# Kernel optimization log

Measured on AMD Instinct MI355X. Metric: run time of the kernel, lower is better.

The kernel has to match this reference:

```python
import jax, jax.numpy as jnp
import numpy as np

N_NODES = 100000
N_EDGES = 1600000
N_GRAPHS = 512


def _graph_conv(x, W, b, src, dst, n_nodes):
    """DGL GraphConv, norm='both': D_in^-1/2 (A (D_out^-1/2 x)) W + b.
    Weight is applied on the smaller-dim side (same math, less memory)."""
    ones = jnp.ones(src.shape[0], dtype=x.dtype)
    deg_out = jnp.clip(jax.ops.segment_sum(ones, src, num_segments=n_nodes), 1.0)
    deg_in = jnp.clip(jax.ops.segment_sum(ones, dst, num_segments=n_nodes), 1.0)
    h = x * (deg_out ** -0.5)[:, None]
    if W.shape[0] > W.shape[1]:  # reduce feature dim before the SpMM
        h = h @ W
        h = jax.ops.segment_sum(h[src], dst, num_segments=n_nodes)
    else:
        h = jax.ops.segment_sum(h[src], dst, num_segments=n_nodes)
        h = h @ W
    return h * (deg_in ** -0.5)[:, None] + b


def setup_inputs() -> dict:
    key = jax.random.key(0)
    ks = jax.random.split(key, 16)
    x = jax.random.normal(ks[0], (N_NODES, 128), dtype=jnp.float32)
    src = jax.random.randint(ks[1], (N_EDGES,), 0, N_NODES, dtype=jnp.int32)
    dst = jax.random.randint(ks[2], (N_EDGES,), 0, N_NODES, dtype=jnp.int32)
    graph_ids = jnp.sort(jax.random.randint(ks[3], (N_NODES,), 0, N_GRAPHS, dtype=jnp.int32))
    s = 0.05
    return {
        "x": x, "src": src, "dst": dst, "graph_ids": graph_ids,
        "W1": jax.random.normal(ks[4], (128, 256), jnp.float32) * s,
        "b1": jnp.zeros((256,), jnp.float32),
        "W2": jax.random.normal(ks[5], (256, 64), jnp.float32) * s,
        "b2": jnp.zeros((64,), jnp.float32),
        "Wc1": jax.random.normal(ks[6], (64, 18), jnp.float32) * s,
        "bc1": jnp.zeros((18,), jnp.float32),
        "Wc2": jax.random.normal(ks[7], (18, 12), jnp.float32) * s,
        "bc2": jnp.zeros((12,), jnp.float32),
        "Wc3": jax.random.normal(ks[8], (12, 6), jnp.float32) * s,
        "bc3": jnp.zeros((6,), jnp.float32),
        "Wc4": jax.random.normal(ks[9], (6, 2), jnp.float32) * s,
        "bc4": jnp.zeros((2,), jnp.float32),
    }


def reference(x, src, dst, graph_ids, W1, b1, W2, b2, Wc1, bc1, Wc2, bc2, Wc3, bc3, Wc4, bc4):
    n = x.shape[0]
    h = jax.nn.relu(_graph_conv(x, W1, b1, src, dst, n))
    h = jax.nn.relu(_graph_conv(h, W2, b2, src, dst, n))
    # dgl.mean_nodes: per-graph mean over nodes
    sums = jax.ops.segment_sum(h, graph_ids, num_segments=N_GRAPHS)
    cnts = jnp.clip(jax.ops.segment_sum(jnp.ones(n, h.dtype), graph_ids, num_segments=N_GRAPHS), 1.0)
    hg = sums / cnts[:, None]
    # classifier: 4 stacked Linear layers, no activations (faithful to source)
    hg = hg @ Wc1 + bc1
    hg = hg @ Wc2 + bc2
    hg = hg @ Wc3 + bc3
    return hg @ Wc4 + bc4
```

## Files before the change

### kernel.cpp

```cpp
#include <hip/hip_runtime.h>
#include <cstdint>
#include <cstddef>

#define NGRAPHS 512

static inline size_t align_up(size_t x, size_t a){ return (x + a - 1) & ~(a - 1); }

__device__ __forceinline__ unsigned short f2bf(float f){
  unsigned int u = __float_as_uint(f);
  u += 0x7FFFu + ((u >> 16) & 1u);
  return (unsigned short)(u >> 16);
}
__device__ __forceinline__ float bflo(unsigned int u){ return __uint_as_float(u << 16); }
__device__ __forceinline__ float bfhi(unsigned int u){ return __uint_as_float(u & 0xffff0000u); }
__device__ __forceinline__ unsigned int pack2(float a, float b){
  return (unsigned)f2bf(a) | ((unsigned)f2bf(b) << 16);
}

typedef __attribute__((ext_vector_type(8))) short bf16x8;
typedef __attribute__((ext_vector_type(4))) float f32x4;

__global__ __launch_bounds__(256) void k_partcount(const int* __restrict__ src, const int* __restrict__ dst,
                                                   int* __restrict__ cntS, int* __restrict__ cntD, int n_edges){
  __shared__ int cs[256], cd[256];
  int tid = threadIdx.x;
  cs[tid] = 0; cd[tid] = 0;
  __syncthreads();
  int e0 = blockIdx.x * 4096;
  int e1 = min(e0 + 4096, n_edges);
  for (int e = e0 + tid; e < e1; e += 256){
    atomicAdd(&cs[src[e] >> 9], 1);
    atomicAdd(&cd[dst[e] >> 9], 1);
  }
  __syncthreads();
  cntS[blockIdx.x * 256 + tid] = cs[tid];
  cntD[blockIdx.x * 256 + tid] = cd[tid];
}

__global__ __launch_bounds__(256) void k_colscan(int* __restrict__ cntS, int* __restrict__ cntD,
                                                 int* __restrict__ totS, int* __restrict__ totD,
                                                 int nblk, int NB){
  int col = blockIdx.x;
  int* cnt; int* tot; int k;
  if (col < NB){ cnt = cntS; tot = totS; k = col; }
  else         { cnt = cntD; tot = totD; k = col - NB; }
  __shared__ int tsum[256];
  int tid = threadIdx.x;
  int i0 = 2 * tid, i1 = 2 * tid + 1;
  int a = (i0 < nblk) ? cnt[i0 * 256 + k] : 0;
  int b = (i1 < nblk) ? cnt[i1 * 256 + k] : 0;
  int s = a + b;
  tsum[tid] = s;
  __syncthreads();
  for (int off = 1; off < 256; off <<= 1){
    int t = (tid >= off) ? tsum[tid - off] : 0;
    __syncthreads();
    tsum[tid] += t;
    __syncthreads();
  }
  int pre = tsum[tid] - s;
  if (i0 < nblk) cnt[i0 * 256 + k] = pre;
  if (i1 < nblk) cnt[i1 * 256 + k] = pre + a;
  if (tid == 255) tot[k] = tsum[255];
}

__global__ __launch_bounds__(256) void k_scatter_det(const int* __restrict__ src, const int* __restrict__ dst,
                                                     const int* __restrict__ cntS, const int* __restrict__ cntD,
                                                     const int* __restrict__ totS, const int* __restrict__ totD,
                                                     int* __restrict__ baseS, int* __restrict__ baseD,
                                                     int2* __restrict__ pairD, int* __restrict__ srcS,
                                                     int n_edges, int NB){
  __shared__ int s1[256], s2[256], curS[256], curD[256];
  int tid = threadIdx.x;
  int b = blockIdx.x;
  int v1 = (tid < NB) ? totS[tid] : 0;
  int v2 = (tid < NB) ? totD[tid] : 0;
  s1[tid] = v1; s2[tid] = v2;
  __syncthreads();
  for (int off = 1; off < 256; off <<= 1){
    int t1 = (tid >= off) ? s1[tid - off] : 0;
    int t2 = (tid >= off) ? s2[tid - off] : 0;
    __syncthreads();
    s1[tid] += t1; s2[tid] += t2;
    __syncthreads();
  }
  int bS = s1[tid] - v1, bD = s2[tid] - v2;
  if (b == 0 && tid < NB){ baseS[tid] = bS; baseD[tid] = bD; }
  curS[tid] = bS + cntS[b * 256 + tid];
  curD[tid] = bD + cntD[b * 256 + tid];
  __syncthreads();
  int e0 = b * 4096, e1 = min(e0 + 4096, n_edges);
  for (int e = e0 + tid; e < e1; e += 256){
    int s = src[e], d = dst[e];
    int pd = atomicAdd(&curD[d >> 9], 1);
    pairD[pd] = make_int2(s, d);
    int ps = atomicAdd(&curS[s >> 9], 1);
    srcS[ps] = s;
  }
}

__global__ __launch_bounds__(256) void k_bucket_build(const int2* __restrict__ pairD, const int* __restrict__ baseD,
                                                      const int* __restrict__ srcS, const int* __restrict__ baseS,
                                                      int* __restrict__ offs, float* __restrict__ din_s,
                                                      float* __restrict__ dout_s, int* __restrict__ csr_src,
                                                      int NB, int n, int n_edges){
  __shared__ int cd[512], cs[512], cur[512];
  __shared__ int tsum[256];
  int b = blockIdx.x, node0 = b << 9, tid = threadIdx.x;
  int nn = min(512, n - node0);
  for (int i = tid; i < 512; i += 256){ cd[i] = 0; cs[i] = 0; }
  __syncthreads();
  int jd0 = baseD[b], jd1 = (b + 1 < NB) ? baseD[b + 1] : n_edges;
  for (int j = jd0 + tid; j < jd1; j += 256) atomicAdd(&cd[pairD[j].y - node0], 1);
  int js0 = baseS[b], js1 = (b + 1 < NB) ? baseS[b + 1] : n_edges;
  for (int j = js0 + tid; j < js1; j += 256) atomicAdd(&cs[srcS[j] - node0], 1);
  __syncthreads();
  int a0 = cd[2 * tid], a1 = cd[2 * tid + 1];
  int s = a0 + a1;
  tsum[tid] = s;
  __syncthreads();
  for (int off = 1; off < 256; off <<= 1){
    int t = (tid >= off) ? tsum[tid - off] : 0;
    __syncthreads();
    tsum[tid] += t;
    __syncthreads();
  }
  int pre = tsum[tid] - s + jd0;
  cur[2 * tid]     = pre;
  cur[2 * tid + 1] = pre + a0;
  __syncthreads();
  for (int i = tid; i < nn; i += 256){
    offs[node0 + i]   = cur[i];
    din_s[node0 + i]  = 1.0f / sqrtf((float)max(cd[i], 1));
    dout_s[node0 + i] = 1.0f / sqrtf((float)max(cs[i], 1));
  }
  if (b == NB - 1 && tid == 0) offs[n] = n_edges;
  __syncthreads();
  for (int j = jd0 + tid; j < jd1; j += 256){
    int2 e = pairD[j];
    int p = atomicAdd(&cur[e.y - node0], 1);
    csr_src[p] = e.x;
  }
}

__global__ __launch_bounds__(256) void k_prep(const float* __restrict__ x, unsigned int* __restrict__ xb,
                                              long long total4,
                                              const float* __restrict__ W1, unsigned short* __restrict__ Wt1,
                                              const float* __restrict__ W2, unsigned short* __restrict__ Wt2,
                                              float* __restrict__ sums,
                                              const int* __restrict__ gids, int* __restrict__ gb, int n_nodes){
  long long t = (long long)blockIdx.x * 256 + threadIdx.x;
  if (t < total4){
    float4 v = ((const float4*)x)[t];
    xb[t * 2 + 0] = pack2(v.x, v.y);
    xb[t * 2 + 1] = pack2(v.z, v.w);
    return;
  }
  long long u = t - total4;
  if (u < 128 * 256){
    int k = (int)(u / 256), n = (int)(u % 256);
    Wt1[(size_t)n * 128 + k] = f2bf(W1[u]);
    return;
  }
  u -= 128 * 256;
  if (u < 256 * 64){
    int k = (int)(u / 64), n = (int)(u % 64);
    Wt2[(size_t)n * 256 + k] = f2bf(W2[u]);
    return;
  }
  u -= 256 * 64;
  if (u < (long long)NGRAPHS * 64){ sums[u] = 0.f; return; }
  u -= (long long)NGRAPHS * 64;
  if (u < n_nodes){
    int i = (int)u;
    int g  = gids[i];
    int gp = (i > 0) ? gids[i - 1] : -1;
    for (int q = gp + 1; q <= g; ++q) gb[q] = i;
    if (i == n_nodes - 1)
      for (int q = g + 1; q <= NGRAPHS; ++q) gb[q] = n_nodes;
  }
}

__global__ __launch_bounds__(256) void k_spmm1(const unsigned int* __restrict__ xb,
    const int* __restrict__ offs, const int* __restrict__ csr_src,
    const float* __restrict__ dout_s, unsigned int* __restrict__ aggb, int n_nodes){
  int node = (blockIdx.x * blockDim.x + threadIdx.x) >> 5;
  int lane = threadIdx.x & 31;
  if (node >= n_nodes) return;
  int j0 = offs[node], j1 = offs[node + 1];
  const uint2* xp = (const uint2*)xb;
  float4 acc = make_float4(0.f, 0.f, 0.f, 0.f);
  int j = j0;
  for (; j + 4 <= j1; j += 4){
    int s0 = csr_src[j + 0];
    int s1 = csr_src[j + 1];
    int s2 = csr_src[j + 2];
    int s3 = csr_src[j + 3];
    float c0 = dout_s[s0];
    float c1 = dout_s[s1];
    float c2 = dout_s[s2];
    float c3 = dout_s[s3];
    uint2 v0 = xp[(size_t)s0 * 32 + lane];
    uint2 v1 = xp[(size_t)s1 * 32 + lane];
    uint2 v2 = xp[(size_t)s2 * 32 + lane];
    uint2 v3 = xp[(size_t)s3 * 32 + lane];
    acc.x = fmaf(bflo(v0.x), c0, acc.x); acc.y = fmaf(bfhi(v0.x), c0, acc.y);
    acc.z = fmaf(bflo(v0.y), c0, acc.z); acc.w = fmaf(bfhi(v0.y), c0, acc.w);
    acc.x = fmaf(bflo(v1.x), c1, acc.x); acc.y = fmaf(bfhi(v1.x), c1, acc.y);
    acc.z = fmaf(bflo(v1.y), c1, acc.z); acc.w = fmaf(bfhi(v1.y), c1, acc.w);
    acc.x = fmaf(bflo(v2.x), c2, acc.x); acc.y = fmaf(bfhi(v2.x), c2, acc.y);
    acc.z = fmaf(bflo(v2.y), c2, acc.z); acc.w = fmaf(bfhi(v2.y), c2, acc.w);
    acc.x = fmaf(bflo(v3.x), c3, acc.x); acc.y = fmaf(bfhi(v3.x), c3, acc.y);
    acc.z = fmaf(bflo(v3.y), c3, acc.z); acc.w = fmaf(bfhi(v3.y), c3, acc.w);
  }
  for (; j < j1; ++j){
    int s = csr_src[j];
    float sc = dout_s[s];
    uint2 v = xp[(size_t)s * 32 + lane];
    acc.x = fmaf(bflo(v.x), sc, acc.x); acc.y = fmaf(bfhi(v.x), sc, acc.y);
    acc.z = fmaf(bflo(v.y), sc, acc.z); acc.w = fmaf(bfhi(v.y), sc, acc.w);
  }
  uint2 pk;
  pk.x = pack2(acc.x, acc.y);
  pk.y = pack2(acc.z, acc.w);
  ((uint2*)aggb)[(size_t)node * 32 + lane] = pk;
}

#define SCHUNK 4
__global__ __launch_bounds__(256) void k_spmm2_fused(const unsigned short* __restrict__ t2,
    const int* __restrict__ offs, const int* __restrict__ csr_src,
    const float* __restrict__ din_s, const float* __restrict__ b2,
    const int* __restrict__ gb, float* __restrict__ sums){
  __shared__ float bs[64];
  int tid = threadIdx.x;
  int g = blockIdx.x & (NGRAPHS - 1);
  int chunk = blockIdx.x >> 9;
  int hw = chunk * 8 + (tid >> 5);
  int lane = tid & 31;
  if (tid < 64) bs[tid] = 0.f;
  __syncthreads();
  int g0 = gb[g], g1 = gb[g + 1];
  const unsigned int* tp = (const unsigned int*)t2;
  float2 bb = ((const float2*)b2)[lane];
  float sx = 0.f, sy = 0.f;
  for (int node = g0 + hw; node < g1; node += 32){
    int j0 = offs[node], j1 = offs[node + 1];
    float ax = 0.f, ay = 0.f;
    int j = j0;
    for (; j + 4 <= j1; j += 4){
      int s0 = csr_src[j + 0];
      int s1 = csr_src[j + 1];
      int s2 = csr_src[j + 2];
      int s3 = csr_src[j + 3];
      unsigned int v0 = tp[(size_t)s0 * 32 + lane];
      unsigned int v1 = tp[(size_t)s1 * 32 + lane];
      unsigned int v2 = tp[(size_t)s2 * 32 + lane];
      unsigned int v3 = tp[(size_t)s3 * 32 + lane];
      ax += bflo(v0) + bflo(v1) + bflo(v2) + bflo(v3);
      ay += bfhi(v0) + bfhi(v1) + bfhi(v2) + bfhi(v3);
    }
    for (; j < j1; ++j){
      unsigned int v = tp[(size_t)csr_src[j] * 32 + lane];
      ax += bflo(v);
      ay += bfhi(v);
    }
    float ds = din_s[node];
    sx += fmaxf(fmaf(ax, ds, bb.x), 0.f);
    sy += fmaxf(fmaf(ay, ds, bb.y), 0.f);
  }
  atomicAdd(&bs[2 * lane], sx);
  atomicAdd(&bs[2 * lane + 1], sy);
  __syncthreads();
  if (tid < 64) atomicAdd(&sums[(size_t)g * 64 + tid], bs[tid]);
}

template<bool C_BF16, bool EPI, bool EPI2>
__global__ __launch_bounds__(256) void gemm_mfma(
    const unsigned short* __restrict__ A, const unsigned short* __restrict__ Bt, void* __restrict__ Cp,
    int M, int N, int K,
    const float* __restrict__ rowScaleC, const float* __restrict__ rowScaleC2,
    const float* __restrict__ bias){
  constexpr int BM = 128, BN = 64, BK = 32, LDA = 40;
  __shared__ __align__(16) unsigned short As[2][BM * LDA];
  __shared__ __align__(16) unsigned short Bs[2][BN * LDA];
  int tid = threadIdx.x;
  int bm0 = blockIdx.x * BM;
  int bn0 = blockIdx.y * BN;
  int wid = tid >> 6, lane = tid & 63;
  int wm = (wid >> 1) * 64, wn = (wid & 1) * 32;
  int quad = lane >> 4, l16 = lane & 15;
  f32x4 acc[4][2];
#pragma unroll
  for (int t = 0; t < 4; ++t)
#pragma unroll
    for (int u = 0; u < 2; ++u) acc[t][u] = f32x4{0.f, 0.f, 0.f, 0.f};

  uint2 ar[4], br[2];
  auto preload = [&](int kk){
#pragma unroll
    for (int it = 0; it < 4; ++it){
      int i = tid + it * 256;
      int m = i >> 3, c = i & 7;
      int gr = bm0 + m;
      ar[it] = (gr < M) ? *(const uint2*)(A + (size_t)gr * K + kk + c * 4) : make_uint2(0u, 0u);
    }
#pragma unroll
    for (int it = 0; it < 2; ++it){
      int i = tid + it * 256;
      int n = i >> 3, c = i & 7;
      br[it] = *(const uint2*)(Bt + (size_t)(bn0 + n) * K + kk + c * 4);
    }
  };
  auto commit = [&](int buf){
#pragma unroll
    for (int it = 0; it < 4; ++it){
      int i = tid + it * 256;
      int m = i >> 3, c = i & 7;
      *(uint2*)&As[buf][m * LDA + c * 4] = ar[it];
    }
#pragma unroll
    for (int it = 0; it < 2; ++it){
      int i = tid + it * 256;
      int n = i >> 3, c = i & 7;
      *(uint2*)&Bs[buf][n * LDA + c * 4] = br[it];
    }
  };

  preload(0);
  commit(0);
  __syncthreads();
  int nk = K / BK;
  for (int kb = 0; kb < nk; ++kb){
    int cur = kb & 1;
    if (kb + 1 < nk) preload((kb + 1) * BK);
    bf16x8 af[4], bfr[2];
#pragma unroll
    for (int t = 0; t < 4; ++t)
      af[t] = *(const bf16x8*)&As[cur][(wm + t * 16 + l16) * LDA + quad * 8];
#pragma unroll
    for (int u = 0; u < 2; ++u)
      bfr[u] = *(const bf16x8*)&Bs[cur][(wn + u * 16 + l16) * LDA + quad * 8];
#pragma unroll
    for (int t = 0; t < 4; ++t)
#pragma unroll
      for (int u = 0; u < 2; ++u)
        acc[t][u] = __builtin_amdgcn_mfma_f32_16x16x32_bf16(af[t], bfr[u], acc[t][u], 0, 0, 0);
    if (kb + 1 < nk){
      commit(cur ^ 1);
      __syncthreads();
    }
  }
  float bv[2] = {0.f, 0.f};
  if constexpr (EPI){ bv[0] = bias[bn0 + wn + l16]; bv[1] = bias[bn0 + wn + 16 + l16]; }
#pragma unroll
  for (int t = 0; t < 4; ++t){
#pragma unroll
    for (int r = 0; r < 4; ++r){
      int gr = bm0 + wm + t * 16 + quad * 4 + r;
      if (gr < M){
        float rs = 1.f, rs2 = 1.f;
        if constexpr (EPI)  rs  = rowScaleC[gr];
        if constexpr (EPI2) rs2 = rowScaleC2[gr];
#pragma unroll
        for (int u = 0; u < 2; ++u){
          int gc = bn0 + wn + u * 16 + l16;
          float cv = acc[t][u][r];
          if constexpr (EPI)  cv = fmaxf(fmaf(cv, rs, bv[u]), 0.f);
          if constexpr (EPI2) cv *= rs2;
          if constexpr (C_BF16) ((unsigned short*)Cp)[(size_t)gr * N + gc] = f2bf(cv);
          else                  ((float*)Cp)[(size_t)gr * N + gc] = cv;
        }
      }
    }
  }
}

__global__ __launch_bounds__(256) void k_classifier(const float* __restrict__ sums, const int* __restrict__ gb,
    const float* __restrict__ Wc1, const float* __restrict__ bc1,
    const float* __restrict__ Wc2, const float* __restrict__ bc2,
    const float* __restrict__ Wc3, const float* __restrict__ bc3,
    const float* __restrict__ Wc4, const float* __restrict__ bc4,
    float* __restrict__ out){
  __shared__ float w1[64 * 18], w2[18 * 12], w3[12 * 6], w4[6 * 2];
  __shared__ float B1[18], B2[12], B3[6], B4[2];
  int tid = threadIdx.x;
  for (int i = tid; i < 64 * 18; i += 256) w1[i] = Wc1[i];
  for (int i = tid; i < 18 * 12; i += 256) w2[i] = Wc2[i];
  for (int i = tid; i < 12 * 6;  i += 256) w3[i] = Wc3[i];
  for (int i = tid; i < 6 * 2;   i += 256) w4[i] = Wc4[i];
  if (tid < 18) B1[tid] = bc1[tid];
  if (tid < 12) B2[tid] = bc2[tid];
  if (tid < 6)  B3[tid] = bc3[tid];
  if (tid < 2)  B4[tid] = bc4[tid];
  __syncthreads();
  int g = blockIdx.x * 256 + tid;
  float cnt = fmaxf((float)(gb[g + 1] - gb[g]), 1.0f);
  float h[64];
#pragma unroll
  for (int f = 0; f < 64; ++f) h[f] = sums[(size_t)g * 64 + f] / cnt;
  float t1[18];
#pragma unroll
  for (int j = 0; j < 18; ++j){
    float s = B1[j];
    for (int f = 0; f < 64; ++f) s = fmaf(h[f], w1[f * 18 + j], s);
    t1[j] = s;
  }
  float t2[12];
#pragma unroll
  for (int j = 0; j < 12; ++j){
    float s = B2[j];
    for (int f = 0; f < 18; ++f) s = fmaf(t1[f], w2[f * 12 + j], s);
    t2[j] = s;
  }
  float t3[6];
#pragma unroll
  for (int j = 0; j < 6; ++j){
    float s = B3[j];
    for (int f = 0; f < 12; ++f) s = fmaf(t2[f], w3[f * 6 + j], s);
    t3[j] = s;
  }
#pragma unroll
  for (int j = 0; j < 2; ++j){
    float s = B4[j];
    for (int f = 0; f < 6; ++f) s = fmaf(t3[f], w4[f * 2 + j], s);
    out[(size_t)g * 2 + j] = s;
  }
}

extern "C" void kernel_launch(void* const* d_in, const int* in_sizes, int n_in,
                              void* d_out, int out_size, void* d_ws, size_t ws_size,
                              hipStream_t stream){
  const float* x   = (const float*)d_in[0];
  const int*   src = (const int*)d_in[1];
  const int*   dst = (const int*)d_in[2];
  const int*   gid = (const int*)d_in[3];
  const float* W1  = (const float*)d_in[4];
  const float* b1  = (const float*)d_in[5];
  const float* W2  = (const float*)d_in[6];
  const float* b2  = (const float*)d_in[7];
  const float* Wc1 = (const float*)d_in[8];
  const float* bc1 = (const float*)d_in[9];
  const float* Wc2 = (const float*)d_in[10];
  const float* bc2 = (const float*)d_in[11];
  const float* Wc3 = (const float*)d_in[12];
  const float* bc3 = (const float*)d_in[13];
  const float* Wc4 = (const float*)d_in[14];
  const float* bc4 = (const float*)d_in[15];
  float* out = (float*)d_out;

  const int n_nodes = in_sizes[3];
  const int n_edges = in_sizes[1];
  const int F1 = 256, F2 = 64;
  const int NB   = (n_nodes + 511) >> 9;
  const int NBLK = (n_edges + 4095) / 4096;

  char* w = (char*)d_ws;
  size_t o = 0;
  auto alloc = [&](size_t bytes) -> char* {
    char* p = w + o;
    o = align_up(o + bytes, 256);
    return p;
  };
  float* sums      = (float*)alloc((size_t)NGRAPHS * F2 * 4);
  int*   gb        = (int*)  alloc((size_t)(NGRAPHS + 1) * 4);
  int*   cntS      = (int*)  alloc((size_t)NBLK * 256 * 4);
  int*   cntD      = (int*)  alloc((size_t)NBLK * 256 * 4);
  int*   totS      = (int*)  alloc((size_t)256 * 4);
  int*   totD      = (int*)  alloc((size_t)256 * 4);
  int*   baseS     = (int*)  alloc((size_t)256 * 4);
  int*   baseD     = (int*)  alloc((size_t)256 * 4);
  float* dout_s    = (float*)alloc((size_t)n_nodes * 4);
  float* din_s     = (float*)alloc((size_t)n_nodes * 4);
  int*   offs      = (int*)  alloc((size_t)(n_nodes + 1) * 4);
  int*   csr_src   = (int*)  alloc((size_t)n_edges * 4);
  unsigned short* Wt1 = (unsigned short*)alloc((size_t)256 * 128 * 2);
  unsigned short* Wt2 = (unsigned short*)alloc((size_t)64 * 256 * 2);
  unsigned int*   xb  = (unsigned int*)  alloc((size_t)n_nodes * 128 * 2);
  unsigned short* aggb= (unsigned short*)alloc((size_t)n_nodes * 128 * 2);
  unsigned short* h1b = (unsigned short*)alloc((size_t)n_nodes * F1 * 2);
  int2*  pairD = (int2*)aggb;
  int*   srcS  = (int*)((char*)aggb + (size_t)n_edges * 8);
  unsigned short* t2b = aggb;

  {
    long long total4 = (long long)n_nodes * 32;
    long long totalP = total4 + 128 * 256 + 256 * 64 + (long long)NGRAPHS * 64 + n_nodes;
    k_prep<<<(int)((totalP + 255) / 256), 256, 0, stream>>>(x, xb, total4, W1, Wt1, W2, Wt2,
                                                            sums, gid, gb, n_nodes);
  }

  k_partcount   <<<NBLK, 256, 0, stream>>>(src, dst, cntS, cntD, n_edges);
  k_colscan     <<<2 * NB, 256, 0, stream>>>(cntS, cntD, totS, totD, NBLK, NB);
  k_scatter_det <<<NBLK, 256, 0, stream>>>(src, dst, cntS, cntD, totS, totD, baseS, baseD, pairD, srcS, n_edges, NB);
  k_bucket_build<<<NB, 256, 0, stream>>>(pairD, baseD, srcS, baseS, offs, din_s, dout_s, csr_src, NB, n_nodes, n_edges);

  int gx = (n_nodes + 127) / 128;
  {
    long long threads = (long long)n_nodes * 32;
    k_spmm1<<<(int)((threads + 255) / 256), 256, 0, stream>>>(xb, offs, csr_src, dout_s, (unsigned int*)aggb, n_nodes);
    gemm_mfma<true, true, true><<<dim3(gx, F1 / 64), 256, 0, stream>>>(
        aggb, Wt1, h1b, n_nodes, F1, 128, din_s, dout_s, b1);
  }
  {
    gemm_mfma<true, false, false><<<dim3(gx, 1), 256, 0, stream>>>(
        h1b, Wt2, t2b, n_nodes, F2, F1, nullptr, nullptr, nullptr);
    k_spmm2_fused<<<NGRAPHS * SCHUNK, 256, 0, stream>>>(t2b, offs, csr_src, din_s, b2, gb, sums);
  }
  k_classifier<<<NGRAPHS / 256, 256, 0, stream>>>(sums, gb, Wc1, bc1, Wc2, bc2, Wc3, bc3, Wc4, bc4, out);
}
```

Measured before the change: 364.9 us.

## Prescale x by out-degree, software-pipeline gathers, add full-N GEMM1 kernel

Moves the weight, sums and graph-boundary prep into the partcount launch and adds a separate prep kernel that converts x to bf16 already multiplied by dout_s. The SpMM1 inner loop then drops the per-edge dout_s gather and FMAs. Both SpMM gathers are unrolled to 8 with the next batch of indices prefetched. A dedicated GEMM1 kernel keeps the A tile in LDS and loops over all four N tiles, so A is loaded once per block rather than per N-block. The costs are an extra launch, rounding x*s to bf16, more registers in the gather loops, and larger LDS use.

```diff
diff --git a/kernel.cpp b/kernel.cpp
--- a/kernel.cpp
+++ b/kernel.cpp
@@ -21,8 +21,38 @@
 typedef __attribute__((ext_vector_type(4))) float f32x4;
 
 __global__ __launch_bounds__(256) void k_partcount(const int* __restrict__ src, const int* __restrict__ dst,
-                                                   int* __restrict__ cntS, int* __restrict__ cntD, int n_edges){
+                                                   int* __restrict__ cntS, int* __restrict__ cntD, int n_edges, int NBLK,
+                                                   const float* __restrict__ W1, unsigned short* __restrict__ Wt1,
+                                                   const float* __restrict__ W2, unsigned short* __restrict__ Wt2,
+                                                   float* __restrict__ sums,
+                                                   const int* __restrict__ gids, int* __restrict__ gb, int n_nodes){
   __shared__ int cs[256], cd[256];
+  if (blockIdx.x >= NBLK){
+    long long u = (long long)(blockIdx.x - NBLK) * 256 + threadIdx.x;
+    if (u < 128 * 256){
+      int k = (int)(u / 256), n = (int)(u % 256);
+      Wt1[(size_t)n * 128 + k] = f2bf(W1[u]);
+      return;
+    }
+    u -= 128 * 256;
+    if (u < 256 * 64){
+      int k = (int)(u / 64), n = (int)(u % 64);
+      Wt2[(size_t)n * 256 + k] = f2bf(W2[u]);
+      return;
+    }
+    u -= 256 * 64;
+    if (u < (long long)NGRAPHS * 64){ sums[u] = 0.f; return; }
+    u -= (long long)NGRAPHS * 64;
+    if (u < n_nodes){
+      int i = (int)u;
+      int g  = gids[i];
+      int gp = (i > 0) ? gids[i - 1] : -1;
+      for (int q = gp + 1; q <= g; ++q) gb[q] = i;
+      if (i == n_nodes - 1)
+        for (int q = g + 1; q <= NGRAPHS; ++q) gb[q] = n_nodes;
+    }
+    return;
+  }
   int tid = threadIdx.x;
   cs[tid] = 0; cd[tid] = 0;
   __syncthreads();
@@ -143,47 +173,20 @@
   }
 }
 
-__global__ __launch_bounds__(256) void k_prep(const float* __restrict__ x, unsigned int* __restrict__ xb,
-                                              long long total4,
-                                              const float* __restrict__ W1, unsigned short* __restrict__ Wt1,
-                                              const float* __restrict__ W2, unsigned short* __restrict__ Wt2,
-                                              float* __restrict__ sums,
-                                              const int* __restrict__ gids, int* __restrict__ gb, int n_nodes){
+__global__ __launch_bounds__(256) void k_prep2(const float* __restrict__ x,
+                                               const float* __restrict__ dout_s,
+                                               unsigned int* __restrict__ xb, long long total4){
   long long t = (long long)blockIdx.x * 256 + threadIdx.x;
-  if (t < total4){
-    float4 v = ((const float4*)x)[t];
-    xb[t * 2 + 0] = pack2(v.x, v.y);
-    xb[t * 2 + 1] = pack2(v.z, v.w);
-    return;
-  }
-  long long u = t - total4;
-  if (u < 128 * 256){
-    int k = (int)(u / 256), n = (int)(u % 256);
-    Wt1[(size_t)n * 128 + k] = f2bf(W1[u]);
-    return;
-  }
-  u -= 128 * 256;
-  if (u < 256 * 64){
-    int k = (int)(u / 64), n = (int)(u % 64);
-    Wt2[(size_t)n * 256 + k] = f2bf(W2[u]);
-    return;
-  }
-  u -= 256 * 64;
-  if (u < (long long)NGRAPHS * 64){ sums[u] = 0.f; return; }
-  u -= (long long)NGRAPHS * 64;
-  if (u < n_nodes){
-    int i = (int)u;
-    int g  = gids[i];
-    int gp = (i > 0) ? gids[i - 1] : -1;
-    for (int q = gp + 1; q <= g; ++q) gb[q] = i;
-    if (i == n_nodes - 1)
-      for (int q = g + 1; q <= NGRAPHS; ++q) gb[q] = n_nodes;
-  }
+  if (t >= total4) return;
+  float4 v = ((const float4*)x)[t];
+  float s = dout_s[t >> 5];
+  xb[t * 2 + 0] = pack2(v.x * s, v.y * s);
+  xb[t * 2 + 1] = pack2(v.z * s, v.w * s);
 }
 
 __global__ __launch_bounds__(256) void k_spmm1(const unsigned int* __restrict__ xb,
     const int* __restrict__ offs, const int* __restrict__ csr_src,
-    const float* __restrict__ dout_s, unsigned int* __restrict__ aggb, int n_nodes){
+    unsigned int* __restrict__ aggb, int n_nodes){
   int node = (blockIdx.x * blockDim.x + threadIdx.x) >> 5;
   int lane = threadIdx.x & 31;
   if (node >= n_nodes) return;
@@ -191,39 +194,151 @@
   const uint2* xp = (const uint2*)xb;
   float4 acc = make_float4(0.f, 0.f, 0.f, 0.f);
   int j = j0;
-  for (; j + 4 <= j1; j += 4){
-    int s0 = csr_src[j + 0];
-    int s1 = csr_src[j + 1];
-    int s2 = csr_src[j + 2];
-    int s3 = csr_src[j + 3];
-    float c0 = dout_s[s0];
-    float c1 = dout_s[s1];
-    float c2 = dout_s[s2];
-    float c3 = dout_s[s3];
-    uint2 v0 = xp[(size_t)s0 * 32 + lane];
-    uint2 v1 = xp[(size_t)s1 * 32 + lane];
-    uint2 v2 = xp[(size_t)s2 * 32 + lane];
-    uint2 v3 = xp[(size_t)s3 * 32 + lane];
-    acc.x = fmaf(bflo(v0.x), c0, acc.x); acc.y = fmaf(bfhi(v0.x), c0, acc.y);
-    acc.z = fmaf(bflo(v0.y), c0, acc.z); acc.w = fmaf(bfhi(v0.y), c0, acc.w);
-    acc.x = fmaf(bflo(v1.x), c1, acc.x); acc.y = fmaf(bfhi(v1.x), c1, acc.y);
-    acc.z = fmaf(bflo(v1.y), c1, acc.z); acc.w = fmaf(bfhi(v1.y), c1, acc.w);
-    acc.x = fmaf(bflo(v2.x), c2, acc.x); acc.y = fmaf(bfhi(v2.x), c2, acc.y);
-    acc.z = fmaf(bflo(v2.y), c2, acc.z); acc.w = fmaf(bfhi(v2.y), c2, acc.w);
-    acc.x = fmaf(bflo(v3.x), c3, acc.x); acc.y = fmaf(bfhi(v3.x), c3, acc.y);
-    acc.z = fmaf(bflo(v3.y), c3, acc.z); acc.w = fmaf(bfhi(v3.y), c3, acc.w);
+  int nfull = (j1 - j0) >> 3;
+  if (nfull > 0){
+    int idx[8];
+#pragma unroll
+    for (int u = 0; u < 8; ++u) idx[u] = csr_src[j + u];
+    for (int b = 0; b < nfull; ++b){
+      int nidx[8];
+      if (b + 1 < nfull){
+#pragma unroll
+        for (int u = 0; u < 8; ++u) nidx[u] = csr_src[j + 8 + u];
+      }
+      uint2 v[8];
+#pragma unroll
+      for (int u = 0; u < 8; ++u) v[u] = xp[(size_t)idx[u] * 32 + lane];
+#pragma unroll
+      for (int u = 0; u < 8; ++u){
+        acc.x += bflo(v[u].x); acc.y += bfhi(v[u].x);
+        acc.z += bflo(v[u].y); acc.w += bfhi(v[u].y);
+      }
+      if (b + 1 < nfull){
+#pragma unroll
+        for (int u = 0; u < 8; ++u) idx[u] = nidx[u];
+      }
+      j += 8;
+    }
   }
   for (; j < j1; ++j){
-    int s = csr_src[j];
-    float sc = dout_s[s];
-    uint2 v = xp[(size_t)s * 32 + lane];
-    acc.x = fmaf(bflo(v.x), sc, acc.x); acc.y = fmaf(bfhi(v.x), sc, acc.y);
-    acc.z = fmaf(bflo(v.y), sc, acc.z); acc.w = fmaf(bfhi(v.y), sc, acc.w);
+    uint2 v = xp[(size_t)csr_src[j] * 32 + lane];
+    acc.x += bflo(v.x); acc.y += bfhi(v.x);
+    acc.z += bflo(v.y); acc.w += bfhi(v.y);
   }
   uint2 pk;
   pk.x = pack2(acc.x, acc.y);
   pk.y = pack2(acc.z, acc.w);
   ((uint2*)aggb)[(size_t)node * 32 + lane] = pk;
+}
+
+__global__ __launch_bounds__(256) void k_gemm1(const unsigned short* __restrict__ A,
+    const unsigned short* __restrict__ Bt, unsigned short* __restrict__ C,
+    int M, const float* __restrict__ din, const float* __restrict__ dout,
+    const float* __restrict__ bias){
+  constexpr int LDA = 136;
+  __shared__ __align__(16) unsigned short As[128 * LDA];
+  __shared__ __align__(16) unsigned short Bs[64 * LDA];
+  int tid = threadIdx.x;
+  int bm0 = blockIdx.x * 128;
+  int wid = tid >> 6, lane = tid & 63;
+  int wm = wid * 32;
+  int quad = lane >> 4, l16 = lane & 15;
+
+  uint4 areg[8];
+#pragma unroll
+  for (int it = 0; it < 8; ++it){
+    int i = tid + it * 256;
+    int m = i >> 4, c = i & 15;
+    int gr = bm0 + m;
+    areg[it] = (gr < M) ? *(const uint4*)(A + (size_t)gr * 128 + c * 8) : make_uint4(0u, 0u, 0u, 0u);
+  }
+  uint4 breg[4];
+#pragma unroll
+  for (int it = 0; it < 4; ++it){
+    int i = tid + it * 256;
+    int n = i >> 4, c = i & 15;
+    breg[it] = *(const uint4*)(Bt + (size_t)n * 128 + c * 8);
+  }
+#pragma unroll
+  for (int it = 0; it < 8; ++it){
+    int i = tid + it * 256;
+    int m = i >> 4, c = i & 15;
+    *(uint4*)&As[m * LDA + c * 8] = areg[it];
+  }
+#pragma unroll
+  for (int it = 0; it < 4; ++it){
+    int i = tid + it * 256;
+    int n = i >> 4, c = i & 15;
+    *(uint4*)&Bs[n * LDA + c * 8] = breg[it];
+  }
+  float rsv[2][4], rs2v[2][4];
+#pragma unroll
+  for (int t = 0; t < 2; ++t)
+#pragma unroll
+    for (int r = 0; r < 4; ++r){
+      int gr = bm0 + wm + t * 16 + quad * 4 + r;
+      rsv[t][r]  = (gr < M) ? din[gr]  : 0.f;
+      rs2v[t][r] = (gr < M) ? dout[gr] : 0.f;
+    }
+  __syncthreads();
+
+  for (int nt = 0; nt < 4; ++nt){
+    if (nt < 3){
+#pragma unroll
+      for (int it = 0; it < 4; ++it){
+        int i = tid + it * 256;
+        int n = i >> 4, c = i & 15;
+        breg[it] = *(const uint4*)(Bt + (size_t)((nt + 1) * 64 + n) * 128 + c * 8);
+      }
+    }
+    f32x4 acc[2][4];
+#pragma unroll
+    for (int t = 0; t < 2; ++t)
+#pragma unroll
+      for (int u = 0; u < 4; ++u) acc[t][u] = f32x4{0.f, 0.f, 0.f, 0.f};
+#pragma unroll
+    for (int ks = 0; ks < 4; ++ks){
+      bf16x8 af[2], bfr[4];
+#pragma unroll
+      for (int t = 0; t < 2; ++t)
+        af[t] = *(const bf16x8*)&As[(wm + t * 16 + l16) * LDA + ks * 32 + quad * 8];
+#pragma unroll
+      for (int u = 0; u < 4; ++u)
+        bfr[u] = *(const bf16x8*)&Bs[(u * 16 + l16) * LDA + ks * 32 + quad * 8];
+#pragma unroll
+      for (int t = 0; t < 2; ++t)
+#pragma unroll
+        for (int u = 0; u < 4; ++u)
+          acc[t][u] = __builtin_amdgcn_mfma_f32_16x16x32_bf16(af[t], bfr[u], acc[t][u], 0, 0, 0);
+    }
+    float bv[4];
+#pragma unroll
+    for (int u = 0; u < 4; ++u) bv[u] = bias[nt * 64 + u * 16 + l16];
+#pragma unroll
+    for (int t = 0; t < 2; ++t){
+#pragma unroll
+      for (int r = 0; r < 4; ++r){
+        int gr = bm0 + wm + t * 16 + quad * 4 + r;
+        if (gr < M){
+#pragma unroll
+          for (int u = 0; u < 4; ++u){
+            float cv = fmaxf(fmaf(acc[t][u][r], rsv[t][r], bv[u]), 0.f) * rs2v[t][r];
+            C[(size_t)gr * 256 + nt * 64 + u * 16 + l16] = f2bf(cv);
+          }
+        }
+      }
+    }
+    if (nt < 3){
+      __syncthreads();
+#pragma unroll
+      for (int it = 0; it < 4; ++it){
+        int i = tid + it * 256;
+        int n = i >> 4, c = i & 15;
+        *(uint4*)&Bs[n * LDA + c * 8] = breg[it];
+      }
+      __syncthreads();
+    }
+  }
 }
 
 #define SCHUNK 4
@@ -247,17 +362,28 @@
     int j0 = offs[node], j1 = offs[node + 1];
     float ax = 0.f, ay = 0.f;
     int j = j0;
-    for (; j + 4 <= j1; j += 4){
-      int s0 = csr_src[j + 0];
-      int s1 = csr_src[j + 1];
-      int s2 = csr_src[j + 2];
-      int s3 = csr_src[j + 3];
-      unsigned int v0 = tp[(size_t)s0 * 32 + lane];
-      unsigned int v1 = tp[(size_t)s1 * 32 + lane];
-      unsigned int v2 = tp[(size_t)s2 * 32 + lane];
-      unsigned int v3 = tp[(size_t)s3 * 32 + lane];
-      ax += bflo(v0) + bflo(v1) + bflo(v2) + bflo(v3);
-      ay += bfhi(v0) + bfhi(v1) + bfhi(v2) + bfhi(v3);
+    int nfull = (j1 - j0) >> 3;
+    if (nfull > 0){
+      int idx[8];
+#pragma unroll
+      for (int u = 0; u < 8; ++u) idx[u] = csr_src[j + u];
+      for (int b = 0; b < nfull; ++b){
+        int nidx[8];
+        if (b + 1 < nfull){
+#pragma unroll
+          for (int u = 0; u < 8; ++u) nidx[u] = csr_src[j + 8 + u];
+        }
+        unsigned int v[8];
+#pragma unroll
+        for (int u = 0; u < 8; ++u) v[u] = tp[(size_t)idx[u] * 32 + lane];
+#pragma unroll
+        for (int u = 0; u < 8; ++u){ ax += bflo(v[u]); ay += bfhi(v[u]); }
+        if (b + 1 < nfull){
+#pragma unroll
+          for (int u = 0; u < 8; ++u) idx[u] = nidx[u];
+        }
+        j += 8;
+      }
     }
     for (; j < j1; ++j){
       unsigned int v = tp[(size_t)csr_src[j] * 32 + lane];
@@ -483,23 +609,25 @@
   unsigned short* t2b = aggb;
 
   {
-    long long total4 = (long long)n_nodes * 32;
-    long long totalP = total4 + 128 * 256 + 256 * 64 + (long long)NGRAPHS * 64 + n_nodes;
-    k_prep<<<(int)((totalP + 255) / 256), 256, 0, stream>>>(x, xb, total4, W1, Wt1, W2, Wt2,
-                                                            sums, gid, gb, n_nodes);
-  }
-
-  k_partcount   <<<NBLK, 256, 0, stream>>>(src, dst, cntS, cntD, n_edges);
+    long long miscTotal = 128 * 256 + 256 * 64 + (long long)NGRAPHS * 64 + n_nodes;
+    int miscBlocks = (int)((miscTotal + 255) / 256);
+    k_partcount<<<NBLK + miscBlocks, 256, 0, stream>>>(src, dst, cntS, cntD, n_edges, NBLK,
+                                                       W1, Wt1, W2, Wt2, sums, gid, gb, n_nodes);
+  }
   k_colscan     <<<2 * NB, 256, 0, stream>>>(cntS, cntD, totS, totD, NBLK, NB);
   k_scatter_det <<<NBLK, 256, 0, stream>>>(src, dst, cntS, cntD, totS, totD, baseS, baseD, pairD, srcS, n_edges, NB);
   k_bucket_build<<<NB, 256, 0, stream>>>(pairD, baseD, srcS, baseS, offs, din_s, dout_s, csr_src, NB, n_nodes, n_edges);
 
+  {
+    long long total4 = (long long)n_nodes * 32;
+    k_prep2<<<(int)((total4 + 255) / 256), 256, 0, stream>>>(x, dout_s, xb, total4);
+  }
+
   int gx = (n_nodes + 127) / 128;
   {
     long long threads = (long long)n_nodes * 32;
-    k_spmm1<<<(int)((threads + 255) / 256), 256, 0, stream>>>(xb, offs, csr_src, dout_s, (unsigned int*)aggb, n_nodes);
-    gemm_mfma<true, true, true><<<dim3(gx, F1 / 64), 256, 0, stream>>>(
-        aggb, Wt1, h1b, n_nodes, F1, 128, din_s, dout_s, b1);
+    k_spmm1<<<(int)((threads + 255) / 256), 256, 0, stream>>>(xb, offs, csr_src, (unsigned int*)aggb, n_nodes);
+    k_gemm1<<<gx, 256, 0, stream>>>(aggb, Wt1, h1b, n_nodes, din_s, dout_s, b1);
   }
   {
     gemm_mfma<true, false, false><<<dim3(gx, 1), 256, 0, stream>>>(
```

Result: no change. 362.4 us (-0.7%).
